# Performance work log

Hardware: AMD Instinct MI355X
Metric: run time of the kernel (lower is better)

The kernel has to match this reference:

```python
import jax, jax.numpy as jnp
import numpy as np

WINDOW = 127          # odd
W = (WINDOW - 1) // 2 # 63 half-window
Q_CH = WINDOW + 1     # 128 query chunk
K_CH = WINDOW * 2     # 254 key chunk


def _compl_mod(m, n):
    return int(n * int(np.ceil(m / n)) - m)


def setup_inputs() -> dict:
    key = jax.random.key(0)
    kq, kk, kv = jax.random.split(key, 3)
    B, L, NH, H = 4, 4096, 16, 64
    return {
        "q": jax.random.normal(kq, (B, L, NH, H), dtype=jnp.float32),
        "k": jax.random.normal(kk, (B, L, NH, H), dtype=jnp.float32),
        "v": jax.random.normal(kv, (B, L, NH, H), dtype=jnp.float32),
    }


def _build_mask(c, k_pad, dtype_bool=bool):
    # base band mask over one (q_ch, k_ch) block: True = masked out
    u = jnp.triu(jnp.ones((Q_CH, K_CH), dtype=bool))
    band = jnp.logical_and(u, jnp.flip(u, (0, 1)))
    base = ~band
    mask_left = base.at[:, :W].set(True)
    mask_right = base.at[:, K_CH - (W + k_pad):].set(True)
    if c > 1:
        mid = jnp.broadcast_to(base, (c - 2, Q_CH, K_CH)) if c > 2 else jnp.zeros((0, Q_CH, K_CH), bool)
        return jnp.concatenate([mask_left[None], mid, mask_right[None]], axis=0)
    return jnp.logical_or(mask_left, mask_right)[None]


def reference(q, k, v):
    b, s, nh, h = q.shape
    q = q * (h ** -0.5)

    q_pad = _compl_mod(s, Q_CH)
    k_pad = _compl_mod(s + 2 * W - K_CH, Q_CH)

    # chunk queries: (b, c, q_ch, nh, h)
    qp = jnp.pad(q, ((0, 0), (0, q_pad), (0, 0), (0, 0)))
    c = (s + q_pad) // Q_CH
    qw = qp.reshape(b, c, Q_CH, nh, h)

    # overlapping key/value windows via gather: (b, c, k_ch, nh, h)
    kp = jnp.pad(k, ((0, 0), (W, W + k_pad), (0, 0), (0, 0)))
    vp = jnp.pad(v, ((0, 0), (W, W + k_pad), (0, 0), (0, 0)))
    starts = np.arange(c) * Q_CH
    idx = starts[:, None] + np.arange(K_CH)[None, :]  # (c, k_ch)
    kw = kp[:, idx]
    vw = vp[:, idx]

    # block scores: (b, nh, c, q_ch, k_ch)
    A = jnp.einsum('bcqnh,bcknh->bncqk', qw, kw)

    mask = _build_mask(c, k_pad)  # (c, q_ch, k_ch)
    neg = -jnp.finfo(A.dtype).max
    A = jnp.where(mask[None, None], neg, A)
    A = jax.nn.softmax(A, axis=-1)

    z = jnp.einsum('bncqk,bcknh->bncqh', A, vw)  # (b, nh, c, q_ch, h)
    z = z.reshape(b, nh, c * Q_CH, h)[:, :, :s]
    return jnp.transpose(z, (0, 2, 1, 3))  # (b, s, nh, h)
```

## Files before the change

kernel.cpp:

```cpp
#include <hip/hip_runtime.h>


typedef _Float16 f16;
typedef _Float16 f16x2  __attribute__((ext_vector_type(2)));
typedef _Float16 f16x4  __attribute__((ext_vector_type(4)));
typedef _Float16 f16x8  __attribute__((ext_vector_type(8)));
typedef float    f32x16 __attribute__((ext_vector_type(16)));
typedef int      int4v  __attribute__((ext_vector_type(4)));

constexpr int NB = 4, L = 4096, NH = 16, H = 64;
constexpr int CQ = 128, NC = L / CQ, KW = 256, WR = 63;
constexpr int RS = NH * H;
constexpr int LDS_BYTES = 32768;

#define DEV static __device__ __forceinline__

DEV int iclamp(int x, int lo, int hi) { return x < lo ? lo : (x > hi ? hi : x); }

DEV float fexp2(float x) {
#if __has_builtin(__builtin_amdgcn_exp2f)
    return __builtin_amdgcn_exp2f(x);
#else
    return exp2f(x);
#endif
}

DEV int packh2(float a, float b) {
    f16x2 p; p.x = (f16)a; p.y = (f16)b;
    return __builtin_bit_cast(int, p);
}

DEV int kaddr(int r, int colb) {
    return r * 128 + (colb ^ ((r & 7) << 4));
}

DEV int vaddr(int h, int kb) {
    return (h * 512 + kb) ^ ((((h & 7) ^ ((h >> 3) & 7))) << 4);
}

DEV void swap_halves(int& a, int& b) {
    asm volatile("v_permlane32_swap_b32 %0, %1" : "+v"(a), "+v"(b));
}

__global__ __launch_bounds__(256, 4)
void wattn_kernel(const float* __restrict__ q_, const float* __restrict__ k_,
                  const float* __restrict__ v_, float* __restrict__ o_)
{
    __shared__ alignas(16) char smem[LDS_BYTES];

    const int bid = (int)blockIdx.x;
    const int wid = (bid & 7) * ((NB * NH * NC) / 8) + (bid >> 3);
    const int c = wid & (NC - 1);
    const int n = (wid >> 5) & (NH - 1);
    const int b = wid >> 9;

    const int t    = (int)threadIdx.x;
    const int lane = t & 63;
    const int w    = t >> 6;
    const int lq   = lane & 31;
    const int hi   = lane >> 5;

    const int kg0 = c * CQ - WR;
    const size_t bn = ((size_t)b * L * NH + n) * H;
    const float qs = 0.125f * 1.44269504088896f;

    const int h4 = (t & 15) << 2;
    const int cb = h4 << 1;
    const int ru = t >> 4;

    const int iq = w * 32 + lq;
    const float* qrow = q_ + bn + (size_t)(c * CQ + iq) * RS + hi * 8;
    f16x8 qf[4];
    #pragma unroll
    for (int tq = 0; tq < 4; ++tq) {
        float4 a  = *(const float4*)(qrow + tq * 16);
        float4 b2 = *(const float4*)(qrow + tq * 16 + 4);
        qf[tq] = (f16x8){(f16)(a.x * qs),  (f16)(a.y * qs),  (f16)(a.z * qs),  (f16)(a.w * qs),
                         (f16)(b2.x * qs), (f16)(b2.y * qs), (f16)(b2.z * qs), (f16)(b2.w * qs)};
    }

    #pragma unroll
    for (int p = 0; p < 16; ++p) {
        int r  = ru + p * 16;
        int kr = iclamp(kg0 + r, 0, L - 1);
        float4 x = *(const float4*)(k_ + bn + (size_t)kr * RS + h4);
        *(f16x4*)(smem + kaddr(r, cb)) = (f16x4){(f16)x.x, (f16)x.y, (f16)x.z, (f16)x.w};
    }

    const int jlo = (c == 0) ? WR : 0;
    const int jhi = (KW < L - kg0) ? KW : (L - kg0);
    const int lo  = (iq > jlo) ? iq : jlo;
    const int hb  = (iq + 126 < jhi - 1) ? (iq + 126) : (jhi - 1);
    const unsigned span = (unsigned)(hb - lo);

    float dsum = 0.f;
    f16x8 pa[5][2];

    __syncthreads();

    #pragma unroll
    for (int i = 0; i < 5; ++i) {
        const int kt = w + i;
        f16x8 kf[4];
        #pragma unroll
        for (int tq = 0; tq < 4; ++tq)
            kf[tq] = *(const f16x8*)(smem + kaddr(kt * 32 + lq, 32 * tq + 16 * hi));

        f32x16 s;
        #pragma unroll
        for (int r = 0; r < 16; ++r) s[r] = 0.f;
        #pragma unroll
        for (int tq = 0; tq < 4; ++tq)
            s = __builtin_amdgcn_mfma_f32_32x32x16_f16(kf[tq], qf[tq], s, 0, 0, 0);

        const int jb = kt * 32 + 4 * hi;
        float pe[16];
        #pragma unroll
        for (int r = 0; r < 16; ++r) {
            int j = jb + (r & 3) + ((r >> 2) << 3);
            float e = fexp2(s[r]);
            e = ((unsigned)(j - lo) <= span) ? e : 0.f;
            dsum += e;
            pe[r] = e;
        }
        int d0 = packh2(pe[0],  pe[1]),  d1 = packh2(pe[2],  pe[3]);
        int d2 = packh2(pe[4],  pe[5]),  d3 = packh2(pe[6],  pe[7]);
        int d4 = packh2(pe[8],  pe[9]),  d5 = packh2(pe[10], pe[11]);
        int d6 = packh2(pe[12], pe[13]), d7 = packh2(pe[14], pe[15]);
        swap_halves(d0, d2); swap_halves(d1, d3);
        swap_halves(d4, d6); swap_halves(d5, d7);
        pa[i][0] = __builtin_bit_cast(f16x8, (int4v){d0, d1, d2, d3});
        pa[i][1] = __builtin_bit_cast(f16x8, (int4v){d4, d5, d6, d7});
    }

    __syncthreads();

    #pragma unroll
    for (int p = 0; p < 8; ++p) {
        int r0  = ru * 2 + p * 32;
        int kr0 = iclamp(kg0 + r0,     0, L - 1);
        int kr1 = iclamp(kg0 + r0 + 1, 0, L - 1);
        float4 v0 = *(const float4*)(v_ + bn + (size_t)kr0 * RS + h4);
        float4 v1 = *(const float4*)(v_ + bn + (size_t)kr1 * RS + h4);
        int kb = r0 * 2;
        *(f16x2*)(smem + vaddr(h4 + 0, kb)) = (f16x2){(f16)v0.x, (f16)v1.x};
        *(f16x2*)(smem + vaddr(h4 + 1, kb)) = (f16x2){(f16)v0.y, (f16)v1.y};
        *(f16x2*)(smem + vaddr(h4 + 2, kb)) = (f16x2){(f16)v0.z, (f16)v1.z};
        *(f16x2*)(smem + vaddr(h4 + 3, kb)) = (f16x2){(f16)v0.w, (f16)v1.w};
    }

    f32x16 o0, o1;
    #pragma unroll
    for (int r = 0; r < 16; ++r) { o0[r] = 0.f; o1[r] = 0.f; }

    __syncthreads();

    #pragma unroll
    for (int i = 0; i < 5; ++i) {
        const int kt = w + i;
        const int kb = kt * 64 + hi * 16;
        f16x8 vb00 = *(const f16x8*)(smem + vaddr(lq,      kb));
        f16x8 vb01 = *(const f16x8*)(smem + vaddr(lq,      kb + 32));
        f16x8 vb10 = *(const f16x8*)(smem + vaddr(32 + lq, kb));
        f16x8 vb11 = *(const f16x8*)(smem + vaddr(32 + lq, kb + 32));
        o0 = __builtin_amdgcn_mfma_f32_32x32x16_f16(vb00, pa[i][0], o0, 0, 0, 0);
        o0 = __builtin_amdgcn_mfma_f32_32x32x16_f16(vb01, pa[i][1], o0, 0, 0, 0);
        o1 = __builtin_amdgcn_mfma_f32_32x32x16_f16(vb10, pa[i][0], o1, 0, 0, 0);
        o1 = __builtin_amdgcn_mfma_f32_32x32x16_f16(vb11, pa[i][1], o1, 0, 0, 0);
    }

    float dtot = dsum + __shfl_xor(dsum, 32, 64);
    float dinv = 1.0f / dtot;
    const size_t ob = ((size_t)b * L + (size_t)c * CQ) * RS + (size_t)n * H;
    float* orow = o_ + ob + (size_t)iq * RS;
    #pragma unroll
    for (int m = 0; m < 4; ++m) {
        int h0 = 8 * m + 4 * hi;
        float4 v0, v1;
        v0.x = o0[4 * m + 0] * dinv;  v0.y = o0[4 * m + 1] * dinv;
        v0.z = o0[4 * m + 2] * dinv;  v0.w = o0[4 * m + 3] * dinv;
        v1.x = o1[4 * m + 0] * dinv;  v1.y = o1[4 * m + 1] * dinv;
        v1.z = o1[4 * m + 2] * dinv;  v1.w = o1[4 * m + 3] * dinv;
        *(float4*)(orow + h0)      = v0;
        *(float4*)(orow + 32 + h0) = v1;
    }
}

extern "C" void kernel_launch(void* const* d_in, const int* in_sizes, int n_in,
                              void* d_out, int out_size, void* d_ws, size_t ws_size,
                              hipStream_t stream) {
    const float* q = (const float*)d_in[0];
    const float* k = (const float*)d_in[1];
    const float* v = (const float*)d_in[2];
    float* o = (float*)d_out;
    (void)in_sizes; (void)n_in; (void)out_size; (void)d_ws; (void)ws_size;
    wattn_kernel<<<dim3(NB * NH * NC), dim3(256), 0, stream>>>(q, k, v, o);
}
```

Baseline: 58.57 us.

## Double query chunk to 256 per block with two-phase K/V staging and fused PV

Each block now handles 256 queries with 512 threads and a 384-row key window. K and V are staged in two phases through a ring of 256 rows in a 64KB LDS buffer. The score and PV MFMAs are fused per key tile, so the probability fragments no longer sit in registers across a barrier. The goal is to cut the redundant halo loads of overlapping K/V windows and the per-block overhead. In exchange it uses more LDS per block, adds barriers, and makes the upper-half warps wait idle during the second load phase.

```diff
diff --git a/kernel.cpp b/kernel.cpp
--- a/kernel.cpp
+++ b/kernel.cpp
@@ -9,9 +9,12 @@
 typedef int      int4v  __attribute__((ext_vector_type(4)));
 
 constexpr int NB = 4, L = 4096, NH = 16, H = 64;
-constexpr int CQ = 128, NC = L / CQ, KW = 256, WR = 63;
+constexpr int CQ = 256, NC = L / CQ, KW = 384, WR = 63;
 constexpr int RS = NH * H;
-constexpr int LDS_BYTES = 32768;
+
+constexpr int K_OFF = 0;
+constexpr int V_OFF = 32768;
+constexpr int LDS_BYTES = 65536;
 
 #define DEV static __device__ __forceinline__
 
@@ -30,19 +33,19 @@
     return __builtin_bit_cast(int, p);
 }
 
-DEV int kaddr(int r, int colb) {
-    return r * 128 + (colb ^ ((r & 7) << 4));
+DEV int kaddr(int rr, int colb) {
+    return K_OFF + rr * 128 + (colb ^ ((rr & 7) << 4));
 }
 
 DEV int vaddr(int h, int kb) {
-    return (h * 512 + kb) ^ ((((h & 7) ^ ((h >> 3) & 7))) << 4);
+    return V_OFF + ((h * 512 + kb) ^ ((((h & 7) ^ ((h >> 3) & 7))) << 4));
 }
 
 DEV void swap_halves(int& a, int& b) {
     asm volatile("v_permlane32_swap_b32 %0, %1" : "+v"(a), "+v"(b));
 }
 
-__global__ __launch_bounds__(256, 4)
+__global__ __launch_bounds__(512, 4)
 void wattn_kernel(const float* __restrict__ q_, const float* __restrict__ k_,
                   const float* __restrict__ v_, float* __restrict__ o_)
 {
@@ -51,8 +54,8 @@
     const int bid = (int)blockIdx.x;
     const int wid = (bid & 7) * ((NB * NH * NC) / 8) + (bid >> 3);
     const int c = wid & (NC - 1);
-    const int n = (wid >> 5) & (NH - 1);
-    const int b = wid >> 9;
+    const int n = (wid >> 4) & (NH - 1);
+    const int b = wid >> 8;
 
     const int t    = (int)threadIdx.x;
     const int lane = t & 63;
@@ -80,11 +83,24 @@
     }
 
     #pragma unroll
-    for (int p = 0; p < 16; ++p) {
-        int r  = ru + p * 16;
+    for (int p = 0; p < 8; ++p) {
+        int r  = ru + p * 32;
         int kr = iclamp(kg0 + r, 0, L - 1);
         float4 x = *(const float4*)(k_ + bn + (size_t)kr * RS + h4);
         *(f16x4*)(smem + kaddr(r, cb)) = (f16x4){(f16)x.x, (f16)x.y, (f16)x.z, (f16)x.w};
+    }
+    #pragma unroll
+    for (int p = 0; p < 4; ++p) {
+        int r0  = ru * 2 + p * 64;
+        int kr0 = iclamp(kg0 + r0,     0, L - 1);
+        int kr1 = iclamp(kg0 + r0 + 1, 0, L - 1);
+        float4 v0 = *(const float4*)(v_ + bn + (size_t)kr0 * RS + h4);
+        float4 v1 = *(const float4*)(v_ + bn + (size_t)kr1 * RS + h4);
+        int kb = r0 * 2;
+        *(f16x2*)(smem + vaddr(h4 + 0, kb)) = (f16x2){(f16)v0.x, (f16)v1.x};
+        *(f16x2*)(smem + vaddr(h4 + 1, kb)) = (f16x2){(f16)v0.y, (f16)v1.y};
+        *(f16x2*)(smem + vaddr(h4 + 2, kb)) = (f16x2){(f16)v0.z, (f16)v1.z};
+        *(f16x2*)(smem + vaddr(h4 + 3, kb)) = (f16x2){(f16)v0.w, (f16)v1.w};
     }
 
     const int jlo = (c == 0) ? WR : 0;
@@ -93,18 +109,17 @@
     const int hb  = (iq + 126 < jhi - 1) ? (iq + 126) : (jhi - 1);
     const unsigned span = (unsigned)(hb - lo);
 
+    f32x16 o0, o1;
+    #pragma unroll
+    for (int r = 0; r < 16; ++r) { o0[r] = 0.f; o1[r] = 0.f; }
     float dsum = 0.f;
-    f16x8 pa[5][2];
-
-    __syncthreads();
-
-    #pragma unroll
-    for (int i = 0; i < 5; ++i) {
-        const int kt = w + i;
+
+    auto body = [&](int kt) {
+        const int rr = (kt & 7) * 32 + lq;
         f16x8 kf[4];
         #pragma unroll
         for (int tq = 0; tq < 4; ++tq)
-            kf[tq] = *(const f16x8*)(smem + kaddr(kt * 32 + lq, 32 * tq + 16 * hi));
+            kf[tq] = *(const f16x8*)(smem + kaddr(rr, 32 * tq + 16 * hi));
 
         f32x16 s;
         #pragma unroll
@@ -129,60 +144,74 @@
         int d6 = packh2(pe[12], pe[13]), d7 = packh2(pe[14], pe[15]);
         swap_halves(d0, d2); swap_halves(d1, d3);
         swap_halves(d4, d6); swap_halves(d5, d7);
-        pa[i][0] = __builtin_bit_cast(f16x8, (int4v){d0, d1, d2, d3});
-        pa[i][1] = __builtin_bit_cast(f16x8, (int4v){d4, d5, d6, d7});
-    }
+        f16x8 pa0 = __builtin_bit_cast(f16x8, (int4v){d0, d1, d2, d3});
+        f16x8 pa1 = __builtin_bit_cast(f16x8, (int4v){d4, d5, d6, d7});
+
+        const int kb = (kt & 7) * 64 + hi * 16;
+        f16x8 vb00 = *(const f16x8*)(smem + vaddr(lq,      kb));
+        f16x8 vb01 = *(const f16x8*)(smem + vaddr(lq,      kb + 32));
+        f16x8 vb10 = *(const f16x8*)(smem + vaddr(32 + lq, kb));
+        f16x8 vb11 = *(const f16x8*)(smem + vaddr(32 + lq, kb + 32));
+        o0 = __builtin_amdgcn_mfma_f32_32x32x16_f16(vb00, pa0, o0, 0, 0, 0);
+        o0 = __builtin_amdgcn_mfma_f32_32x32x16_f16(vb01, pa1, o0, 0, 0, 0);
+        o1 = __builtin_amdgcn_mfma_f32_32x32x16_f16(vb10, pa0, o1, 0, 0, 0);
+        o1 = __builtin_amdgcn_mfma_f32_32x32x16_f16(vb11, pa1, o1, 0, 0, 0);
+    };
+
+    auto epilogue = [&]() {
+        float dtot = dsum + __shfl_xor(dsum, 32, 64);
+        float dinv = 1.0f / dtot;
+        const size_t ob = ((size_t)b * L + (size_t)c * CQ) * RS + (size_t)n * H;
+        float* orow = o_ + ob + (size_t)iq * RS;
+        #pragma unroll
+        for (int m = 0; m < 4; ++m) {
+            int h0 = 8 * m + 4 * hi;
+            float4 v0, v1;
+            v0.x = o0[4 * m + 0] * dinv;  v0.y = o0[4 * m + 1] * dinv;
+            v0.z = o0[4 * m + 2] * dinv;  v0.w = o0[4 * m + 3] * dinv;
+            v1.x = o1[4 * m + 0] * dinv;  v1.y = o1[4 * m + 1] * dinv;
+            v1.z = o1[4 * m + 2] * dinv;  v1.w = o1[4 * m + 3] * dinv;
+            *(float4*)(orow + h0)      = v0;
+            *(float4*)(orow + 32 + h0) = v1;
+        }
+    };
 
     __syncthreads();
 
-    #pragma unroll
-    for (int p = 0; p < 8; ++p) {
-        int r0  = ru * 2 + p * 32;
+    {
+        const int kend = (w + 4 < 7) ? (w + 4) : 7;
+        for (int kt = w; kt <= kend; ++kt) body(kt);
+    }
+    if (w < 4) epilogue();
+
+    __syncthreads();
+
+    #pragma unroll
+    for (int p = 0; p < 4; ++p) {
+        int r  = 256 + ru + p * 32;
+        int kr = iclamp(kg0 + r, 0, L - 1);
+        float4 x = *(const float4*)(k_ + bn + (size_t)kr * RS + h4);
+        *(f16x4*)(smem + kaddr(r - 256, cb)) = (f16x4){(f16)x.x, (f16)x.y, (f16)x.z, (f16)x.w};
+    }
+    #pragma unroll
+    for (int p = 0; p < 2; ++p) {
+        int r0  = 256 + ru * 2 + p * 64;
         int kr0 = iclamp(kg0 + r0,     0, L - 1);
         int kr1 = iclamp(kg0 + r0 + 1, 0, L - 1);
         float4 v0 = *(const float4*)(v_ + bn + (size_t)kr0 * RS + h4);
         float4 v1 = *(const float4*)(v_ + bn + (size_t)kr1 * RS + h4);
-        int kb = r0 * 2;
+        int kb = (r0 - 256) * 2;
         *(f16x2*)(smem + vaddr(h4 + 0, kb)) = (f16x2){(f16)v0.x, (f16)v1.x};
         *(f16x2*)(smem + vaddr(h4 + 1, kb)) = (f16x2){(f16)v0.y, (f16)v1.y};
         *(f16x2*)(smem + vaddr(h4 + 2, kb)) = (f16x2){(f16)v0.z, (f16)v1.z};
         *(f16x2*)(smem + vaddr(h4 + 3, kb)) = (f16x2){(f16)v0.w, (f16)v1.w};
     }
 
-    f32x16 o0, o1;
-    #pragma unroll
-    for (int r = 0; r < 16; ++r) { o0[r] = 0.f; o1[r] = 0.f; }
-
     __syncthreads();
 
-    #pragma unroll
-    for (int i = 0; i < 5; ++i) {
-        const int kt = w + i;
-        const int kb = kt * 64 + hi * 16;
-        f16x8 vb00 = *(const f16x8*)(smem + vaddr(lq,      kb));
-        f16x8 vb01 = *(const f16x8*)(smem + vaddr(lq,      kb + 32));
-        f16x8 vb10 = *(const f16x8*)(smem + vaddr(32 + lq, kb));
-        f16x8 vb11 = *(const f16x8*)(smem + vaddr(32 + lq, kb + 32));
-        o0 = __builtin_amdgcn_mfma_f32_32x32x16_f16(vb00, pa[i][0], o0, 0, 0, 0);
-        o0 = __builtin_amdgcn_mfma_f32_32x32x16_f16(vb01, pa[i][1], o0, 0, 0, 0);
-        o1 = __builtin_amdgcn_mfma_f32_32x32x16_f16(vb10, pa[i][0], o1, 0, 0, 0);
-        o1 = __builtin_amdgcn_mfma_f32_32x32x16_f16(vb11, pa[i][1], o1, 0, 0, 0);
-    }
-
-    float dtot = dsum + __shfl_xor(dsum, 32, 64);
-    float dinv = 1.0f / dtot;
-    const size_t ob = ((size_t)b * L + (size_t)c * CQ) * RS + (size_t)n * H;
-    float* orow = o_ + ob + (size_t)iq * RS;
-    #pragma unroll
-    for (int m = 0; m < 4; ++m) {
-        int h0 = 8 * m + 4 * hi;
-        float4 v0, v1;
-        v0.x = o0[4 * m + 0] * dinv;  v0.y = o0[4 * m + 1] * dinv;
-        v0.z = o0[4 * m + 2] * dinv;  v0.w = o0[4 * m + 3] * dinv;
-        v1.x = o1[4 * m + 0] * dinv;  v1.y = o1[4 * m + 1] * dinv;
-        v1.z = o1[4 * m + 2] * dinv;  v1.w = o1[4 * m + 3] * dinv;
-        *(float4*)(orow + h0)      = v0;
-        *(float4*)(orow + 32 + h0) = v1;
+    if (w >= 4) {
+        for (int kt = 8; kt <= w + 4; ++kt) body(kt);
+        epilogue();
     }
 }
 
@@ -194,5 +223,5 @@
     const float* v = (const float*)d_in[2];
     float* o = (float*)d_out;
     (void)in_sizes; (void)n_in; (void)out_size; (void)d_ws; (void)ws_size;
-    wattn_kernel<<<dim3(NB * NH * NC), dim3(256), 0, stream>>>(q, k, v, o);
-}
+    wattn_kernel<<<dim3(NB * NH * NC), dim3(512), 0, stream>>>(q, k, v, o);
+}
```

After: 55.02 us. -6.0%, faster.

## Halve query chunk and split key tiles across warp pairs with LDS reduction

Applied to the files above, without the earlier changes.

Query chunks shrink from 128 to 64 rows, which doubles the number of blocks, and the key window shrinks to 192. Each pair of warps splits that query tile's key tiles (3 and 2), and the partial outputs and denominators are combined through LDS. K and V are now staged into LDS together up front, and the score and PV steps are fused per tile, removing the register array of probabilities and one barrier. The cost is more redundant K/V loading per query, since window overlap grows relative to chunk size, plus a larger LDS footprint (48KB, launch bounds lowered to 3) and extra reduction traffic.

```diff
diff --git a/kernel.cpp b/kernel.cpp
--- a/kernel.cpp
+++ b/kernel.cpp
@@ -9,9 +9,15 @@
 typedef int      int4v  __attribute__((ext_vector_type(4)));
 
 constexpr int NB = 4, L = 4096, NH = 16, H = 64;
-constexpr int CQ = 128, NC = L / CQ, KW = 256, WR = 63;
+constexpr int CQ = 64, NC = L / CQ, KW = 192, WR = 63;
+constexpr int NBLK = NB * NH * NC;
 constexpr int RS = NH * H;
-constexpr int LDS_BYTES = 32768;
+
+constexpr int K_OFF = 0;
+constexpr int V_OFF = 24576;
+constexpr int X_OFF = 0;
+constexpr int D_OFF = 16384;
+constexpr int LDS_BYTES = 49152;
 
 #define DEV static __device__ __forceinline__
 
@@ -31,34 +37,38 @@
 }
 
 DEV int kaddr(int r, int colb) {
-    return r * 128 + (colb ^ ((r & 7) << 4));
+    return K_OFF + r * 128 + (colb ^ ((r & 7) << 4));
 }
 
 DEV int vaddr(int h, int kb) {
-    return (h * 512 + kb) ^ ((((h & 7) ^ ((h >> 3) & 7))) << 4);
+    return V_OFF + ((h * 384 + kb) ^ ((((h & 7) ^ ((h >> 3) & 7))) << 4));
 }
 
 DEV void swap_halves(int& a, int& b) {
     asm volatile("v_permlane32_swap_b32 %0, %1" : "+v"(a), "+v"(b));
 }
 
-__global__ __launch_bounds__(256, 4)
+__global__ __launch_bounds__(256, 3)
 void wattn_kernel(const float* __restrict__ q_, const float* __restrict__ k_,
                   const float* __restrict__ v_, float* __restrict__ o_)
 {
     __shared__ alignas(16) char smem[LDS_BYTES];
+    float* X_lds = (float*)(smem + X_OFF);
+    float* D_lds = (float*)(smem + D_OFF);
 
     const int bid = (int)blockIdx.x;
-    const int wid = (bid & 7) * ((NB * NH * NC) / 8) + (bid >> 3);
+    const int wid = (bid & 7) * (NBLK / 8) + (bid >> 3);
     const int c = wid & (NC - 1);
-    const int n = (wid >> 5) & (NH - 1);
-    const int b = wid >> 9;
+    const int n = (wid >> 6) & (NH - 1);
+    const int b = wid >> 10;
 
     const int t    = (int)threadIdx.x;
     const int lane = t & 63;
     const int w    = t >> 6;
     const int lq   = lane & 31;
     const int hi   = lane >> 5;
+    const int qt   = w & 1;
+    const int part = w >> 1;
 
     const int kg0 = c * CQ - WR;
     const size_t bn = ((size_t)b * L * NH + n) * H;
@@ -68,7 +78,7 @@
     const int cb = h4 << 1;
     const int ru = t >> 4;
 
-    const int iq = w * 32 + lq;
+    const int iq = qt * 32 + lq;
     const float* qrow = q_ + bn + (size_t)(c * CQ + iq) * RS + hi * 8;
     f16x8 qf[4];
     #pragma unroll
@@ -80,11 +90,24 @@
     }
 
     #pragma unroll
-    for (int p = 0; p < 16; ++p) {
+    for (int p = 0; p < 12; ++p) {
         int r  = ru + p * 16;
         int kr = iclamp(kg0 + r, 0, L - 1);
         float4 x = *(const float4*)(k_ + bn + (size_t)kr * RS + h4);
         *(f16x4*)(smem + kaddr(r, cb)) = (f16x4){(f16)x.x, (f16)x.y, (f16)x.z, (f16)x.w};
+    }
+    #pragma unroll
+    for (int p = 0; p < 6; ++p) {
+        int r0  = ru * 2 + p * 32;
+        int kr0 = iclamp(kg0 + r0,     0, L - 1);
+        int kr1 = iclamp(kg0 + r0 + 1, 0, L - 1);
+        float4 v0 = *(const float4*)(v_ + bn + (size_t)kr0 * RS + h4);
+        float4 v1 = *(const float4*)(v_ + bn + (size_t)kr1 * RS + h4);
+        int kb = r0 * 2;
+        *(f16x2*)(smem + vaddr(h4 + 0, kb)) = (f16x2){(f16)v0.x, (f16)v1.x};
+        *(f16x2*)(smem + vaddr(h4 + 1, kb)) = (f16x2){(f16)v0.y, (f16)v1.y};
+        *(f16x2*)(smem + vaddr(h4 + 2, kb)) = (f16x2){(f16)v0.z, (f16)v1.z};
+        *(f16x2*)(smem + vaddr(h4 + 3, kb)) = (f16x2){(f16)v0.w, (f16)v1.w};
     }
 
     const int jlo = (c == 0) ? WR : 0;
@@ -93,18 +116,18 @@
     const int hb  = (iq + 126 < jhi - 1) ? (iq + 126) : (jhi - 1);
     const unsigned span = (unsigned)(hb - lo);
 
+    f32x16 o0, o1;
+    #pragma unroll
+    for (int r = 0; r < 16; ++r) { o0[r] = 0.f; o1[r] = 0.f; }
     float dsum = 0.f;
-    f16x8 pa[5][2];
 
     __syncthreads();
 
-    #pragma unroll
-    for (int i = 0; i < 5; ++i) {
-        const int kt = w + i;
+    auto body = [&](int tl) {
         f16x8 kf[4];
         #pragma unroll
         for (int tq = 0; tq < 4; ++tq)
-            kf[tq] = *(const f16x8*)(smem + kaddr(kt * 32 + lq, 32 * tq + 16 * hi));
+            kf[tq] = *(const f16x8*)(smem + kaddr(tl * 32 + lq, 32 * tq + 16 * hi));
 
         f32x16 s;
         #pragma unroll
@@ -113,7 +136,7 @@
         for (int tq = 0; tq < 4; ++tq)
             s = __builtin_amdgcn_mfma_f32_32x32x16_f16(kf[tq], qf[tq], s, 0, 0, 0);
 
-        const int jb = kt * 32 + 4 * hi;
+        const int jb = tl * 32 + 4 * hi;
         float pe[16];
         #pragma unroll
         for (int r = 0; r < 16; ++r) {
@@ -129,60 +152,59 @@
         int d6 = packh2(pe[12], pe[13]), d7 = packh2(pe[14], pe[15]);
         swap_halves(d0, d2); swap_halves(d1, d3);
         swap_halves(d4, d6); swap_halves(d5, d7);
-        pa[i][0] = __builtin_bit_cast(f16x8, (int4v){d0, d1, d2, d3});
-        pa[i][1] = __builtin_bit_cast(f16x8, (int4v){d4, d5, d6, d7});
-    }
-
-    __syncthreads();
-
-    #pragma unroll
-    for (int p = 0; p < 8; ++p) {
-        int r0  = ru * 2 + p * 32;
-        int kr0 = iclamp(kg0 + r0,     0, L - 1);
-        int kr1 = iclamp(kg0 + r0 + 1, 0, L - 1);
-        float4 v0 = *(const float4*)(v_ + bn + (size_t)kr0 * RS + h4);
-        float4 v1 = *(const float4*)(v_ + bn + (size_t)kr1 * RS + h4);
-        int kb = r0 * 2;
-        *(f16x2*)(smem + vaddr(h4 + 0, kb)) = (f16x2){(f16)v0.x, (f16)v1.x};
-        *(f16x2*)(smem + vaddr(h4 + 1, kb)) = (f16x2){(f16)v0.y, (f16)v1.y};
-        *(f16x2*)(smem + vaddr(h4 + 2, kb)) = (f16x2){(f16)v0.z, (f16)v1.z};
-        *(f16x2*)(smem + vaddr(h4 + 3, kb)) = (f16x2){(f16)v0.w, (f16)v1.w};
-    }
-
-    f32x16 o0, o1;
-    #pragma unroll
-    for (int r = 0; r < 16; ++r) { o0[r] = 0.f; o1[r] = 0.f; }
-
-    __syncthreads();
-
-    #pragma unroll
-    for (int i = 0; i < 5; ++i) {
-        const int kt = w + i;
-        const int kb = kt * 64 + hi * 16;
+        f16x8 pa0 = __builtin_bit_cast(f16x8, (int4v){d0, d1, d2, d3});
+        f16x8 pa1 = __builtin_bit_cast(f16x8, (int4v){d4, d5, d6, d7});
+
+        const int kb = tl * 64 + hi * 16;
         f16x8 vb00 = *(const f16x8*)(smem + vaddr(lq,      kb));
         f16x8 vb01 = *(const f16x8*)(smem + vaddr(lq,      kb + 32));
         f16x8 vb10 = *(const f16x8*)(smem + vaddr(32 + lq, kb));
         f16x8 vb11 = *(const f16x8*)(smem + vaddr(32 + lq, kb + 32));
-        o0 = __builtin_amdgcn_mfma_f32_32x32x16_f16(vb00, pa[i][0], o0, 0, 0, 0);
-        o0 = __builtin_amdgcn_mfma_f32_32x32x16_f16(vb01, pa[i][1], o0, 0, 0, 0);
-        o1 = __builtin_amdgcn_mfma_f32_32x32x16_f16(vb10, pa[i][0], o1, 0, 0, 0);
-        o1 = __builtin_amdgcn_mfma_f32_32x32x16_f16(vb11, pa[i][1], o1, 0, 0, 0);
-    }
-
-    float dtot = dsum + __shfl_xor(dsum, 32, 64);
-    float dinv = 1.0f / dtot;
-    const size_t ob = ((size_t)b * L + (size_t)c * CQ) * RS + (size_t)n * H;
-    float* orow = o_ + ob + (size_t)iq * RS;
-    #pragma unroll
-    for (int m = 0; m < 4; ++m) {
-        int h0 = 8 * m + 4 * hi;
-        float4 v0, v1;
-        v0.x = o0[4 * m + 0] * dinv;  v0.y = o0[4 * m + 1] * dinv;
-        v0.z = o0[4 * m + 2] * dinv;  v0.w = o0[4 * m + 3] * dinv;
-        v1.x = o1[4 * m + 0] * dinv;  v1.y = o1[4 * m + 1] * dinv;
-        v1.z = o1[4 * m + 2] * dinv;  v1.w = o1[4 * m + 3] * dinv;
-        *(float4*)(orow + h0)      = v0;
-        *(float4*)(orow + 32 + h0) = v1;
+        o0 = __builtin_amdgcn_mfma_f32_32x32x16_f16(vb00, pa0, o0, 0, 0, 0);
+        o0 = __builtin_amdgcn_mfma_f32_32x32x16_f16(vb01, pa1, o0, 0, 0, 0);
+        o1 = __builtin_amdgcn_mfma_f32_32x32x16_f16(vb10, pa0, o1, 0, 0, 0);
+        o1 = __builtin_amdgcn_mfma_f32_32x32x16_f16(vb11, pa1, o1, 0, 0, 0);
+    };
+
+    const int kt0 = qt + part * 3;
+    body(kt0);
+    body(kt0 + 1);
+    if (!part) body(kt0 + 2);
+
+    float dw = dsum + __shfl_xor(dsum, 32, 64);
+
+    __syncthreads();
+
+    if (part) {
+        #pragma unroll
+        for (int r = 0; r < 16; ++r) {
+            int h = (r & 3) + ((r >> 2) << 3) + 4 * hi;
+            X_lds[h * 64 + iq]        = o0[r];
+            X_lds[(32 + h) * 64 + iq] = o1[r];
+        }
+        if (lane < 32) D_lds[iq] = dw;
+    }
+    __syncthreads();
+
+    if (!part) {
+        float dinv = 1.0f / (dw + D_lds[iq]);
+        const size_t ob = ((size_t)b * L + (size_t)c * CQ) * RS + (size_t)n * H;
+        float* orow = o_ + ob + (size_t)iq * RS;
+        #pragma unroll
+        for (int m = 0; m < 4; ++m) {
+            int h0 = 8 * m + 4 * hi;
+            float4 v0, v1;
+            v0.x = (o0[4 * m + 0] + X_lds[(h0 + 0) * 64 + iq]) * dinv;
+            v0.y = (o0[4 * m + 1] + X_lds[(h0 + 1) * 64 + iq]) * dinv;
+            v0.z = (o0[4 * m + 2] + X_lds[(h0 + 2) * 64 + iq]) * dinv;
+            v0.w = (o0[4 * m + 3] + X_lds[(h0 + 3) * 64 + iq]) * dinv;
+            v1.x = (o1[4 * m + 0] + X_lds[(32 + h0 + 0) * 64 + iq]) * dinv;
+            v1.y = (o1[4 * m + 1] + X_lds[(32 + h0 + 1) * 64 + iq]) * dinv;
+            v1.z = (o1[4 * m + 2] + X_lds[(32 + h0 + 2) * 64 + iq]) * dinv;
+            v1.w = (o1[4 * m + 3] + X_lds[(32 + h0 + 3) * 64 + iq]) * dinv;
+            *(float4*)(orow + h0)      = v0;
+            *(float4*)(orow + 32 + h0) = v1;
+        }
     }
 }
 
@@ -194,5 +216,5 @@
     const float* v = (const float*)d_in[2];
     float* o = (float*)d_out;
     (void)in_sizes; (void)n_in; (void)out_size; (void)d_ws; (void)ws_size;
-    wattn_kernel<<<dim3(NB * NH * NC), dim3(256), 0, stream>>>(q, k, v, o);
-}
+    wattn_kernel<<<dim3(NBLK), dim3(256), 0, stream>>>(q, k, v, o);
+}
```

Result: faster. 52.56 us (-10.3%).
